# Optimization experiments

Hardware: AMD Instinct MI355X
Metric: run time of the kernel (lower is better)

Reference implementation:

```python
import jax, jax.numpy as jnp
import numpy as np

N_NODES = 20000
N_EDGES = 320000
INDIM = 64
OUTDIM = 128
EDGE_DIM = 16
HEADS = 4
ED = OUTDIM // 2          # encoded edge dim = 64
C1 = 2 * INDIM // HEADS   # 32 -> concat 128
C2 = OUTDIM // HEADS      # 32 -> concat 128
C3 = 2 * OUTDIM // HEADS  # 64 -> concat 256


def setup_inputs() -> dict:
    key = jax.random.key(0)
    ks = iter(jax.random.split(key, 80))
    def p(*shape):
        return jax.random.normal(next(ks), shape, dtype=jnp.float32) * 0.05
    inp = {}
    inp['x_in'] = jax.random.normal(next(ks), (N_NODES, INDIM), dtype=jnp.float32)
    inp['edge_index'] = jax.random.randint(next(ks), (2, N_EDGES), 0, N_NODES)
    inp['edge_attr'] = jax.random.normal(next(ks), (N_EDGES, EDGE_DIM), dtype=jnp.float32)
    # BatchNorm1d (eval mode: running stats)
    inp['bn0_g'] = jnp.ones(INDIM, jnp.float32) + p(INDIM)
    inp['bn0_b'] = p(INDIM)
    inp['bn0_m'] = p(INDIM)
    inp['bn0_v'] = jnp.ones(INDIM, jnp.float32) + 0.1 * jax.random.uniform(next(ks), (INDIM,))
    # edge encoder: Linear(edge_dim,outdim) -> LeakyReLU -> Linear(outdim,outdim//2) -> LeakyReLU
    inp['ee_W1'] = p(EDGE_DIM, OUTDIM); inp['ee_b1'] = p(OUTDIM)
    inp['ee_W2'] = p(OUTDIM, ED); inp['ee_b2'] = p(ED)
    # GATv2 layers: lin_l, lin_r (bias), lin_edge (no bias), att [H,C], out bias [H*C]
    def gat_params(prefix, din, C):
        inp[prefix + '_Wl'] = p(din, HEADS * C); inp[prefix + '_bl'] = p(HEADS * C)
        inp[prefix + '_Wr'] = p(din, HEADS * C); inp[prefix + '_br'] = p(HEADS * C)
        inp[prefix + '_We'] = p(ED, HEADS * C)
        inp[prefix + '_att'] = p(HEADS, C)
        inp[prefix + '_bias'] = p(HEADS * C)
    gat_params('g1', INDIM, C1)
    gat_params('g2', HEADS * C1, C2)
    gat_params('g3', HEADS * C2, C3)
    # LayerNorms
    inp['ln1_g'] = jnp.ones(HEADS * C1, jnp.float32); inp['ln1_b'] = p(HEADS * C1)
    inp['ln2_g'] = jnp.ones(HEADS * C2, jnp.float32); inp['ln2_b'] = p(HEADS * C2)
    inp['ln3_g'] = jnp.ones(HEADS * C3, jnp.float32); inp['ln3_b'] = p(HEADS * C3)
    # skip / mixing / heads
    inp['skip_W'] = p(INDIM, HEADS * C1); inp['skip_b'] = p(HEADS * C1)
    inp['alpha_p'] = jnp.float32(0.3)
    inp['fp_W'] = p(HEADS * C1, HEADS * C3); inp['fp_b'] = p(HEADS * C3)
    catout = HEADS * C3
    inp['np_W1'] = p(catout, catout // 2); inp['np_b1'] = p(catout // 2)
    inp['np_W2'] = p(catout // 2, catout // 4); inp['np_b2'] = p(catout // 4)
    inp['np_W3'] = p(catout // 4, 1); inp['np_b3'] = p(1)
    return inp


def _ln(x, g, b):
    m = jnp.mean(x, axis=-1, keepdims=True)
    v = jnp.var(x, axis=-1, keepdims=True)
    return (x - m) / jnp.sqrt(v + 1e-5) * g + b


def _gatv2(x, src, dst, ea, Wl, bl, Wr, br, We, att, bias, N):
    # GATv2Conv (eval): e = att . leaky_relu(x_j + x_i + e_ij, 0.2); segment softmax over dst
    H, C = att.shape
    xl = (x @ Wl + bl).reshape(N, H, C)   # source transform
    xr = (x @ Wr + br).reshape(N, H, C)   # target transform
    ee = (ea @ We).reshape(-1, H, C)      # edge transform (no bias)
    m = jax.nn.leaky_relu(xl[src] + xr[dst] + ee, 0.2)  # [E,H,C]
    e = jnp.einsum('ehc,hc->eh', m, att)
    emax = jax.ops.segment_max(e, dst, num_segments=N)
    ex = jnp.exp(e - emax[dst])
    den = jax.ops.segment_sum(ex, dst, num_segments=N)
    alpha = ex / (den[dst] + 1e-16)       # [E,H]
    out = jax.ops.segment_sum(xl[src] * alpha[:, :, None], dst, num_segments=N)
    return out.reshape(N, H * C) + bias, alpha


def reference(x_in, edge_index, edge_attr, bn0_g, bn0_b, bn0_m, bn0_v,
              ee_W1, ee_b1, ee_W2, ee_b2,
              g1_Wl, g1_bl, g1_Wr, g1_br, g1_We, g1_att, g1_bias,
              g2_Wl, g2_bl, g2_Wr, g2_br, g2_We, g2_att, g2_bias,
              g3_Wl, g3_bl, g3_Wr, g3_br, g3_We, g3_att, g3_bias,
              ln1_g, ln1_b, ln2_g, ln2_b, ln3_g, ln3_b,
              skip_W, skip_b, alpha_p, fp_W, fp_b,
              np_W1, np_b1, np_W2, np_b2, np_W3, np_b3):
    N = x_in.shape[0]
    # BatchNorm1d eval
    x = (x_in - bn0_m) / jnp.sqrt(bn0_v + 1e-5) * bn0_g + bn0_b
    # edge encoder + L2 normalize
    ea = jax.nn.leaky_relu(edge_attr @ ee_W1 + ee_b1, 0.01)
    ea = jax.nn.leaky_relu(ea @ ee_W2 + ee_b2, 0.01)
    ea = ea / jnp.maximum(jnp.linalg.norm(ea, axis=-1, keepdims=True), 1e-12)
    # add self loops (fill_value='mean' of incoming encoded edge_attr)
    src0, dst0 = edge_index[0], edge_index[1]
    deg = jax.ops.segment_sum(jnp.ones_like(ea[:, 0]), dst0, num_segments=N)
    loop_attr = jax.ops.segment_sum(ea, dst0, num_segments=N) / jnp.maximum(deg, 1.0)[:, None]
    ar = jnp.arange(N, dtype=src0.dtype)
    src = jnp.concatenate([src0, ar]); dst = jnp.concatenate([dst0, ar])
    ea2 = jnp.concatenate([ea, loop_attr], axis=0)
    x1, a1 = _gatv2(x, src, dst, ea2, g1_Wl, g1_bl, g1_Wr, g1_br, g1_We, g1_att, g1_bias, N)
    x1 = jax.nn.leaky_relu(_ln(x1, ln1_g, ln1_b), 0.01)
    skip1 = 0.01 * (x @ skip_W + skip_b) + x1  # skip_weight = 0.01 (frozen)
    x2, a2 = _gatv2(skip1, src, dst, ea2, g2_Wl, g2_bl, g2_Wr, g2_br, g2_We, g2_att, g2_bias, N)
    x2 = jax.nn.leaky_relu(_ln(x2, ln2_g, ln2_b), 0.01)
    x3, a3 = _gatv2(x2, src, dst, ea2, g3_Wl, g3_bl, g3_Wr, g3_br, g3_We, g3_att, g3_bias, N)
    x3 = jax.nn.leaky_relu(_ln(x3, ln3_g, ln3_b), 0.01)
    s = jax.nn.sigmoid(alpha_p)
    xf = s * (x1 @ fp_W + fp_b) + (1.0 - s) * x3
    h = jax.nn.elu(xf @ np_W1 + np_b1)
    h = jax.nn.elu(h @ np_W2 + np_b2)
    node_probs = h @ np_W3 + np_b3
    return (xf, node_probs, a1, a2, a3)
```

## Files before the change

### kernel.cpp

```cpp
#include <hip/hip_runtime.h>
#include <math.h>

#define DEV __device__ __forceinline__

typedef __attribute__((ext_vector_type(8))) short bf16x8;
typedef __attribute__((ext_vector_type(4))) float f32x4;

DEV float leakyf(float x, float s) { return x > 0.f ? x : s * x; }

DEV unsigned short f2bf(float f) {
  unsigned u = __float_as_uint(f);
  unsigned r = (u + 0x7fff + ((u >> 16) & 1)) >> 16;
  return (unsigned short)r;
}
DEV float bf2f(unsigned short h) { return __uint_as_float((unsigned)h << 16); }

DEV float sel4(float4 v, int h) {
  float a = (h & 1) ? v.y : v.x;
  float b = (h & 1) ? v.w : v.z;
  return (h & 2) ? b : a;
}

DEV float wave_sum(float v) {
#pragma unroll
  for (int o = 1; o < 64; o <<= 1) v += __shfl_xor(v, o);
  return v;
}
DEV float wave_max(float v) {
#pragma unroll
  for (int o = 1; o < 64; o <<= 1) v = fmaxf(v, __shfl_xor(v, o));
  return v;
}

struct WJob { const float* in; unsigned short* out; int K; int Nc; };
struct WJobs { WJob j[13]; };

__global__ __launch_bounds__(256) void wt_kernel(WJobs jobs) {
  WJob jb = jobs.j[blockIdx.y];
  int total = jb.K * jb.Nc;
  for (int i = blockIdx.x * 256 + threadIdx.x; i < total; i += gridDim.x * 256) {
    int c = i / jb.K, k = i - c * jb.K;
    jb.out[i] = f2bf(jb.in[(size_t)k * jb.Nc + c]);
  }
}

__global__ __launch_bounds__(256) void bn_kernel(
    const float* __restrict__ xin, const float* __restrict__ g,
    const float* __restrict__ b, const float* __restrict__ m,
    const float* __restrict__ v, float* __restrict__ xout, int total) {
  int i = blockIdx.x * 256 + threadIdx.x;
  if (i < total) {
    int c = i & 63;
    xout[i] = (xin[i] - m[c]) * rsqrtf(v[c] + 1e-5f) * g[c] + b[c];
  }
}

__global__ __launch_bounds__(256, 2) void edge_enc_kernel(
    const float* __restrict__ edge_attr, const unsigned short* __restrict__ WT1,
    const float* __restrict__ b1, const unsigned short* __restrict__ WT2,
    const float* __restrict__ b2, unsigned short* __restrict__ ea_bf, int E) {
  __shared__ unsigned short sEa1[64][136];
  int tid = threadIdx.x, lane = tid & 63, w = tid >> 6;
  int g = lane >> 4, q = lane & 15;
  bf16x8 w1f[8];
#pragma unroll
  for (int t = 0; t < 8; t++) {
    bf16x8 v = {};
    if (g < 2) v = *(const bf16x8*)(WT1 + (size_t)(16 * t + q) * 16 + 8 * g);
    w1f[t] = v;
  }
  float b1v[8];
#pragma unroll
  for (int t = 0; t < 8; t++) b1v[t] = b1[16 * t + q];
  bf16x8 w2f[4][4];
#pragma unroll
  for (int t = 0; t < 4; t++)
#pragma unroll
    for (int kc = 0; kc < 4; kc++)
      w2f[t][kc] = *(const bf16x8*)(WT2 + (size_t)(16 * t + q) * 128 + 32 * kc + 8 * g);
  float b2v[4];
#pragma unroll
  for (int t = 0; t < 4; t++) b2v[t] = b2[16 * t + q];

  int gstride = gridDim.x * 64;

  auto load_attr = [&](int base) -> bf16x8 {
    bf16x8 af = {};
    if (g < 2) {
      int e = base + w * 16 + q;
      if (e >= E) e = E - 1;
      const float* ap = edge_attr + (size_t)e * 16 + 8 * g;
      float4 x0 = *(const float4*)ap;
      float4 x1 = *(const float4*)(ap + 4);
      af[0] = (short)f2bf(x0.x); af[1] = (short)f2bf(x0.y);
      af[2] = (short)f2bf(x0.z); af[3] = (short)f2bf(x0.w);
      af[4] = (short)f2bf(x1.x); af[5] = (short)f2bf(x1.y);
      af[6] = (short)f2bf(x1.z); af[7] = (short)f2bf(x1.w);
    }
    return af;
  };

  int base = blockIdx.x * 64;
  if (base >= E) return;
  bf16x8 af = load_attr(base);
  for (; base < E; ) {
    int next = base + gstride;
    bf16x8 af_next = {};
    if (next < E) af_next = load_attr(next);
    int e0 = base + w * 16;
    f32x4 acc1[8];
#pragma unroll
    for (int t = 0; t < 8; t++) acc1[t] = (f32x4){0.f, 0.f, 0.f, 0.f};
#pragma unroll
    for (int t = 0; t < 8; t++)
      acc1[t] = __builtin_amdgcn_mfma_f32_16x16x32_bf16(af, w1f[t], acc1[t], 0, 0, 0);
#pragma unroll
    for (int t = 0; t < 8; t++)
#pragma unroll
      for (int r = 0; r < 4; r++) {
        float v = leakyf(acc1[t][r] + b1v[t], 0.01f);
        sEa1[w * 16 + g * 4 + r][16 * t + q] = f2bf(v);
      }
    f32x4 acc2[4];
#pragma unroll
    for (int t = 0; t < 4; t++) acc2[t] = (f32x4){0.f, 0.f, 0.f, 0.f};
#pragma unroll
    for (int kc = 0; kc < 4; kc++) {
      bf16x8 a2 = *(const bf16x8*)&sEa1[w * 16 + q][32 * kc + 8 * g];
#pragma unroll
      for (int t = 0; t < 4; t++)
        acc2[t] = __builtin_amdgcn_mfma_f32_16x16x32_bf16(a2, w2f[t][kc], acc2[t], 0, 0, 0);
    }
#pragma unroll
    for (int r = 0; r < 4; r++) {
      float vv[4];
      float p = 0.f;
#pragma unroll
      for (int t = 0; t < 4; t++) {
        float v = leakyf(acc2[t][r] + b2v[t], 0.01f);
        vv[t] = v;
        p += v * v;
      }
#pragma unroll
      for (int o = 1; o < 16; o <<= 1) p += __shfl_xor(p, o);
      float sc = 1.f / fmaxf(sqrtf(p), 1e-12f);
      int e = e0 + g * 4 + r;
      if (e < E) {
#pragma unroll
        for (int t = 0; t < 4; t++)
          ea_bf[(size_t)e * 64 + 16 * t + q] = f2bf(vv[t] * sc);
      }
    }
    af = af_next;
    base = next;
  }
}

__global__ __launch_bounds__(256) void count_kernel(const int* __restrict__ dst0,
                                                    int* __restrict__ counts, int E, int E2) {
  int i = blockIdx.x * 256 + threadIdx.x;
  if (i < E2) {
    int d = (i < E) ? dst0[i] : (i - E);
    atomicAdd(&counts[d], 1);
  }
}

__global__ __launch_bounds__(1024) void scan_kernel(const int* __restrict__ counts,
                                                    int* __restrict__ rowptr,
                                                    int* __restrict__ fill, int N) {
  __shared__ int part[1024];
  int tid = threadIdx.x;
  int chunk = (N + 1023) / 1024;
  int lo = tid * chunk, hi = lo + chunk;
  if (hi > N) hi = N;
  if (lo > N) lo = N;
  int s = 0;
  for (int i = lo; i < hi; i++) s += counts[i];
  part[tid] = s;
  __syncthreads();
#pragma unroll
  for (int o = 1; o < 1024; o <<= 1) {
    int v = (tid >= o) ? part[tid - o] : 0;
    __syncthreads();
    part[tid] += v;
    __syncthreads();
  }
  if (tid == 1023) rowptr[N] = part[1023];
  int off = part[tid] - s;
  for (int i = lo; i < hi; i++) {
    rowptr[i] = off;
    fill[i] = off;
    off += counts[i];
  }
}

__global__ __launch_bounds__(256) void fill_kernel(const int* __restrict__ src0,
                                                   const int* __restrict__ dst0,
                                                   int* __restrict__ fill,
                                                   int* __restrict__ csr,
                                                   int* __restrict__ srcpos,
                                                   int* __restrict__ dstpos, int E, int E2) {
  int i = blockIdx.x * 256 + threadIdx.x;
  if (i < E2) {
    int d, s;
    if (i < E) {
      d = dst0[i];
      s = src0[i];
    } else {
      d = s = i - E;
    }
    int pos = atomicAdd(&fill[d], 1);
    csr[pos] = i;
    srcpos[pos] = s;
    dstpos[pos] = d;
  }
}

__global__ __launch_bounds__(256) void loopattr_kernel(unsigned short* __restrict__ ea_bf,
                                                       const int* __restrict__ rowptr,
                                                       const int* __restrict__ csr, int N, int E) {
  int lane = threadIdx.x & 63, wv = threadIdx.x >> 6;
  int stride = gridDim.x * 4;
  for (int n = blockIdx.x * 4 + wv; n < N; n += stride) {
    int r0 = rowptr[n], r1 = rowptr[n + 1];
    float acc = 0.f;
    int cnt = 0;
    for (int i = r0; i < r1; i++) {
      int e = csr[i];
      if (e < E) {
        acc += bf2f(ea_bf[(size_t)e * 64 + lane]);
        cnt++;
      }
    }
    ea_bf[((size_t)E + n) * 64 + lane] = f2bf(acc / fmaxf((float)cnt, 1.f));
  }
}

template <int MODE>
__global__ __launch_bounds__(256) void gemm_mfma_kernel(
    const float* __restrict__ A, const unsigned short* __restrict__ BT,
    const float* __restrict__ bias, void* __restrict__ Cout, int M, int K, int Nc,
    const float* __restrict__ aux, const float* __restrict__ alpha_p) {
  __shared__ unsigned short sA[64][40];
  __shared__ unsigned short sB[64][40];
  int tid = threadIdx.x, lane = tid & 63, w = tid >> 6;
  int g = lane >> 4, q = lane & 15;
  int bm = blockIdx.y * 64, bn = blockIdx.x * 64;
  f32x4 acc[4];
#pragma unroll
  for (int t = 0; t < 4; t++) acc[t] = (f32x4){0.f, 0.f, 0.f, 0.f};
  int r = tid >> 2, ko = (tid & 3) * 8;
  for (int k0 = 0; k0 < K; k0 += 32) {
    {
      int gm = bm + r;
      bf16x8 v = {};
      if (gm < M) {
        const float* ap = A + (size_t)gm * K + k0 + ko;
        float4 x0 = *(const float4*)ap;
        float4 x1 = *(const float4*)(ap + 4);
        v[0] = (short)f2bf(x0.x); v[1] = (short)f2bf(x0.y);
        v[2] = (short)f2bf(x0.z); v[3] = (short)f2bf(x0.w);
        v[4] = (short)f2bf(x1.x); v[5] = (short)f2bf(x1.y);
        v[6] = (short)f2bf(x1.z); v[7] = (short)f2bf(x1.w);
      }
      *(bf16x8*)&sA[r][ko] = v;
      int gc = bn + r;
      bf16x8 bv = {};
      if (gc < Nc) bv = *(const bf16x8*)(BT + (size_t)gc * K + k0 + ko);
      *(bf16x8*)&sB[r][ko] = bv;
    }
    __syncthreads();
    bf16x8 a = *(const bf16x8*)&sA[w * 16 + q][8 * g];
#pragma unroll
    for (int t = 0; t < 4; t++) {
      bf16x8 b = *(const bf16x8*)&sB[16 * t + q][8 * g];
      acc[t] = __builtin_amdgcn_mfma_f32_16x16x32_bf16(a, b, acc[t], 0, 0, 0);
    }
    __syncthreads();
  }
  float s = 0.f;
  if (MODE == 3) s = 1.f / (1.f + __expf(-alpha_p[0]));
#pragma unroll
  for (int t = 0; t < 4; t++) {
    int col = bn + 16 * t + q;
#pragma unroll
    for (int rr = 0; rr < 4; rr++) {
      int row = bm + w * 16 + g * 4 + rr;
      if (row < M && col < Nc) {
        float v = acc[t][rr] + bias[col];
        if (MODE == 2) v = v > 0.f ? v : (__expf(v) - 1.f);
        if (MODE == 3) v = s * v + (1.f - s) * aux[(size_t)row * Nc + col];
        if (MODE == 1)
          ((unsigned short*)Cout)[(size_t)row * Nc + col] = f2bf(v);
        else
          ((float*)Cout)[(size_t)row * Nc + col] = v;
      }
    }
  }
}

struct GJob { const unsigned short* BT; const float* bias; void* out; int mode; };
struct GJobs { GJob j[3]; };

__global__ __launch_bounds__(256) void gemm_mfma_batched(
    const float* __restrict__ A, GJobs jobs, int M, int K, int Nc) {
  __shared__ unsigned short sA[64][40];
  __shared__ unsigned short sB[64][40];
  GJob jb = jobs.j[blockIdx.z];
  const unsigned short* BT = jb.BT;
  int tid = threadIdx.x, lane = tid & 63, w = tid >> 6;
  int g = lane >> 4, q = lane & 15;
  int bm = blockIdx.y * 64, bn = blockIdx.x * 64;
  f32x4 acc[4];
#pragma unroll
  for (int t = 0; t < 4; t++) acc[t] = (f32x4){0.f, 0.f, 0.f, 0.f};
  int r = tid >> 2, ko = (tid & 3) * 8;
  for (int k0 = 0; k0 < K; k0 += 32) {
    {
      int gm = bm + r;
      bf16x8 v = {};
      if (gm < M) {
        const float* ap = A + (size_t)gm * K + k0 + ko;
        float4 x0 = *(const float4*)ap;
        float4 x1 = *(const float4*)(ap + 4);
        v[0] = (short)f2bf(x0.x); v[1] = (short)f2bf(x0.y);
        v[2] = (short)f2bf(x0.z); v[3] = (short)f2bf(x0.w);
        v[4] = (short)f2bf(x1.x); v[5] = (short)f2bf(x1.y);
        v[6] = (short)f2bf(x1.z); v[7] = (short)f2bf(x1.w);
      }
      *(bf16x8*)&sA[r][ko] = v;
      int gc = bn + r;
      bf16x8 bv = {};
      if (gc < Nc) bv = *(const bf16x8*)(BT + (size_t)gc * K + k0 + ko);
      *(bf16x8*)&sB[r][ko] = bv;
    }
    __syncthreads();
    bf16x8 a = *(const bf16x8*)&sA[w * 16 + q][8 * g];
#pragma unroll
    for (int t = 0; t < 4; t++) {
      bf16x8 b = *(const bf16x8*)&sB[16 * t + q][8 * g];
      acc[t] = __builtin_amdgcn_mfma_f32_16x16x32_bf16(a, b, acc[t], 0, 0, 0);
    }
    __syncthreads();
  }
#pragma unroll
  for (int t = 0; t < 4; t++) {
    int col = bn + 16 * t + q;
#pragma unroll
    for (int rr = 0; rr < 4; rr++) {
      int row = bm + w * 16 + g * 4 + rr;
      if (row < M && col < Nc) {
        float v = acc[t][rr] + jb.bias[col];
        if (jb.mode == 1)
          ((unsigned short*)jb.out)[(size_t)row * Nc + col] = f2bf(v);
        else
          ((float*)jb.out)[(size_t)row * Nc + col] = v;
      }
    }
  }
}

template <int C, bool SPLIT>
__global__ __launch_bounds__(256) void score_mfma_kernel(
    const unsigned short* __restrict__ ea_bf, const unsigned short* __restrict__ xl,
    const unsigned short* __restrict__ xr, const float* __restrict__ We,
    const float* __restrict__ att, const int* __restrict__ csr,
    const int* __restrict__ srcpos, const int* __restrict__ dstpos,
    float* __restrict__ e_s, int E2, int HCfull, int col_off_in) {
  int lane = threadIdx.x & 63;
  int wv = threadIdx.x >> 6;
  int g = lane >> 4, q = lane & 15;
  int col_off = SPLIT ? (wv & 1) * 128 : col_off_in;
  bf16x8 bfrag[8][2];
#pragma unroll
  for (int t = 0; t < 8; t++)
#pragma unroll
    for (int kc = 0; kc < 2; kc++) {
      bf16x8 bv;
#pragma unroll
      for (int j = 0; j < 8; j++) {
        int k = kc * 32 + g * 8 + j;
        bv[j] = (short)f2bf(We[(size_t)k * HCfull + col_off + 16 * t + q]);
      }
      bfrag[t][kc] = bv;
    }
  float attv[8];
#pragma unroll
  for (int t = 0; t < 8; t++) attv[t] = att[col_off + 16 * t + q];

  constexpr int TPH = C / 16;
  constexpr int NH = 8 / TPH;
  const int headbase = col_off / C;

  int tiles = (E2 + 15) / 16;
  int tstart = SPLIT ? (blockIdx.x * 2 + (wv >> 1)) : (blockIdx.x * 4 + wv);
  int nw = SPLIT ? (gridDim.x * 2) : (gridDim.x * 4);
  for (int tile = tstart; tile < tiles; tile += nw) {
    int i0 = tile * 16;
    int ia = i0 + q;
    if (ia >= E2) ia = E2 - 1;
    int erow = csr[ia];
    const unsigned short* ap = ea_bf + (size_t)erow * 64 + g * 8;
    bf16x8 a0 = *(const bf16x8*)(ap);
    bf16x8 a1 = *(const bf16x8*)(ap + 32);
    f32x4 acc[8];
#pragma unroll
    for (int t = 0; t < 8; t++) acc[t] = (f32x4){0.f, 0.f, 0.f, 0.f};
#pragma unroll
    for (int t = 0; t < 8; t++) {
      acc[t] = __builtin_amdgcn_mfma_f32_16x16x32_bf16(a0, bfrag[t][0], acc[t], 0, 0, 0);
      acc[t] = __builtin_amdgcn_mfma_f32_16x16x32_bf16(a1, bfrag[t][1], acc[t], 0, 0, 0);
    }
    int sn[4], dn[4];
#pragma unroll
    for (int r = 0; r < 4; r++) {
      int i = i0 + g * 4 + r;
      if (i >= E2) i = E2 - 1;
      sn[r] = srcpos[i];
      dn[r] = dstpos[i];
    }
    float p[NH][4];
#pragma unroll
    for (int hh = 0; hh < NH; hh++)
#pragma unroll
      for (int r = 0; r < 4; r++) p[hh][r] = 0.f;
#pragma unroll
    for (int t = 0; t < 8; t++) {
      int col = col_off + 16 * t + q;
#pragma unroll
      for (int r = 0; r < 4; r++) {
        float xv = bf2f(xl[(size_t)sn[r] * HCfull + col]) +
                   bf2f(xr[(size_t)dn[r] * HCfull + col]) + acc[t][r];
        xv = xv > 0.f ? xv : 0.2f * xv;
        p[t / TPH][r] += xv * attv[t];
      }
    }
#pragma unroll
    for (int hh = 0; hh < NH; hh++)
#pragma unroll
      for (int r = 0; r < 4; r++) {
#pragma unroll
        for (int o = 1; o < 16; o <<= 1) p[hh][r] += __shfl_xor(p[hh][r], o);
      }
    if (q == 0) {
#pragma unroll
      for (int r = 0; r < 4; r++) {
        int i = i0 + g * 4 + r;
        if (i < E2) {
#pragma unroll
          for (int hh = 0; hh < NH; hh++)
            e_s[(size_t)i * 4 + headbase + hh] = p[hh][r];
        }
      }
    }
  }
}

template <int HC, bool L1MODE>
__global__ __launch_bounds__(256) void aggr_kernel(
    const float* __restrict__ e_s, const unsigned short* __restrict__ xl,
    const int* __restrict__ rowptr, const int* __restrict__ srcpos,
    const float* __restrict__ bias,
    const float* __restrict__ lng, const float* __restrict__ lnb,
    float* __restrict__ xout,
    float* __restrict__ x1out, const float* __restrict__ skipproj,
    float* __restrict__ md, int N) {
  constexpr int CPL = HC / 64;
  int lane = threadIdx.x & 63, wv = threadIdx.x >> 6;
  int stride = gridDim.x * 4;
  const float4* e_s4 = (const float4*)e_s;
  for (int n = blockIdx.x * 4 + wv; n < N; n += stride) {
    int r0 = rowptr[n], r1 = rowptr[n + 1];
    float m0 = -1e30f, m1 = -1e30f, m2 = -1e30f, m3 = -1e30f;
    for (int i = r0 + lane; i < r1; i += 64) {
      float4 v = e_s4[i];
      m0 = fmaxf(m0, v.x);
      m1 = fmaxf(m1, v.y);
      m2 = fmaxf(m2, v.z);
      m3 = fmaxf(m3, v.w);
    }
    m0 = wave_max(m0);
    m1 = wave_max(m1);
    m2 = wave_max(m2);
    m3 = wave_max(m3);
    float d0 = 0.f, d1 = 0.f, d2 = 0.f, d3 = 0.f;
    for (int i = r0 + lane; i < r1; i += 64) {
      float4 v = e_s4[i];
      d0 += __expf(v.x - m0);
      d1 += __expf(v.y - m1);
      d2 += __expf(v.z - m2);
      d3 += __expf(v.w - m3);
    }
    d0 = wave_sum(d0);
    d1 = wave_sum(d1);
    d2 = wave_sum(d2);
    d3 = wave_sum(d3);
    float i0 = 1.f / (d0 + 1e-16f), i1 = 1.f / (d1 + 1e-16f);
    float i2 = 1.f / (d2 + 1e-16f), i3 = 1.f / (d3 + 1e-16f);
    if (lane == 0) {
      float* mp = md + (size_t)n * 8;
      mp[0] = m0; mp[1] = m1; mp[2] = m2; mp[3] = m3;
      mp[4] = i0; mp[5] = i1; mp[6] = i2; mp[7] = i3;
    }
    int h = lane >> 4;
    float mh = (h & 2) ? ((h & 1) ? m3 : m2) : ((h & 1) ? m1 : m0);
    float ih = (h & 2) ? ((h & 1) ? i3 : i2) : ((h & 1) ? i1 : i0);
    float acc[CPL];
#pragma unroll
    for (int j = 0; j < CPL; j++) acc[j] = 0.f;
    int c0 = lane * CPL;
    int i = r0;
    for (; i + 4 <= r1; i += 4) {
      float sh0, sh1, sh2, sh3;
      int sn0, sn1, sn2, sn3;
      {
        float4 a = e_s4[i], b = e_s4[i + 1], c = e_s4[i + 2], d = e_s4[i + 3];
        sh0 = sel4(a, h); sh1 = sel4(b, h); sh2 = sel4(c, h); sh3 = sel4(d, h);
      }
      sn0 = srcpos[i]; sn1 = srcpos[i + 1]; sn2 = srcpos[i + 2]; sn3 = srcpos[i + 3];
      if constexpr (CPL == 2) {
        ushort2 t0 = *(const ushort2*)(xl + (size_t)sn0 * HC + c0);
        ushort2 t1 = *(const ushort2*)(xl + (size_t)sn1 * HC + c0);
        ushort2 t2 = *(const ushort2*)(xl + (size_t)sn2 * HC + c0);
        ushort2 t3 = *(const ushort2*)(xl + (size_t)sn3 * HC + c0);
        float a0 = __expf(sh0 - mh) * ih;
        float a1 = __expf(sh1 - mh) * ih;
        float a2 = __expf(sh2 - mh) * ih;
        float a3 = __expf(sh3 - mh) * ih;
        acc[0] += a0 * bf2f(t0.x) + a1 * bf2f(t1.x) + a2 * bf2f(t2.x) + a3 * bf2f(t3.x);
        acc[1] += a0 * bf2f(t0.y) + a1 * bf2f(t1.y) + a2 * bf2f(t2.y) + a3 * bf2f(t3.y);
      } else {
        ushort4 t0 = *(const ushort4*)(xl + (size_t)sn0 * HC + c0);
        ushort4 t1 = *(const ushort4*)(xl + (size_t)sn1 * HC + c0);
        ushort4 t2 = *(const ushort4*)(xl + (size_t)sn2 * HC + c0);
        ushort4 t3 = *(const ushort4*)(xl + (size_t)sn3 * HC + c0);
        float a0 = __expf(sh0 - mh) * ih;
        float a1 = __expf(sh1 - mh) * ih;
        float a2 = __expf(sh2 - mh) * ih;
        float a3 = __expf(sh3 - mh) * ih;
        acc[0] += a0 * bf2f(t0.x) + a1 * bf2f(t1.x) + a2 * bf2f(t2.x) + a3 * bf2f(t3.x);
        acc[1] += a0 * bf2f(t0.y) + a1 * bf2f(t1.y) + a2 * bf2f(t2.y) + a3 * bf2f(t3.y);
        acc[2] += a0 * bf2f(t0.z) + a1 * bf2f(t1.z) + a2 * bf2f(t2.z) + a3 * bf2f(t3.z);
        acc[3] += a0 * bf2f(t0.w) + a1 * bf2f(t1.w) + a2 * bf2f(t2.w) + a3 * bf2f(t3.w);
      }
    }
    for (; i < r1; i++) {
      float sh = sel4(e_s4[i], h);
      float a = __expf(sh - mh) * ih;
      int sn = srcpos[i];
      const unsigned short* xp = xl + (size_t)sn * HC + c0;
      if constexpr (CPL == 2) {
        ushort2 t = *(const ushort2*)xp;
        acc[0] += a * bf2f(t.x);
        acc[1] += a * bf2f(t.y);
      } else {
        ushort4 t = *(const ushort4*)xp;
        acc[0] += a * bf2f(t.x);
        acc[1] += a * bf2f(t.y);
        acc[2] += a * bf2f(t.z);
        acc[3] += a * bf2f(t.w);
      }
    }
    float vals[CPL];
    float vs = 0.f, vq = 0.f;
#pragma unroll
    for (int j = 0; j < CPL; j++) {
      float t = acc[j] + bias[c0 + j];
      vals[j] = t;
      vs += t;
      vq += t * t;
    }
    vs = wave_sum(vs);
    vq = wave_sum(vq);
    float mean = vs * (1.f / HC);
    float var = vq * (1.f / HC) - mean * mean;
    float rstd = rsqrtf(fmaxf(var, 0.f) + 1e-5f);
#pragma unroll
    for (int j = 0; j < CPL; j++) {
      int c = c0 + j;
      float y = (vals[j] - mean) * rstd * lng[c] + lnb[c];
      y = leakyf(y, 0.01f);
      if constexpr (L1MODE) {
        x1out[(size_t)n * HC + c] = y;
        xout[(size_t)n * HC + c] = 0.01f * skipproj[(size_t)n * HC + c] + y;
      } else {
        xout[(size_t)n * HC + c] = y;
      }
    }
  }
}

__global__ __launch_bounds__(256) void alpha_kernel(
    const float* __restrict__ e_s, const int* __restrict__ csr,
    const int* __restrict__ dstpos, const float* __restrict__ md,
    float* __restrict__ alpha_out, int E2) {
  int i = blockIdx.x * 256 + threadIdx.x;
  if (i < E2) {
    float4 sv = ((const float4*)e_s)[i];
    int d = dstpos[i];
    const float* mp = md + (size_t)d * 8;
    float4 a;
    a.x = __expf(sv.x - mp[0]) * mp[4];
    a.y = __expf(sv.y - mp[1]) * mp[5];
    a.z = __expf(sv.z - mp[2]) * mp[6];
    a.w = __expf(sv.w - mp[3]) * mp[7];
    ((float4*)alpha_out)[csr[i]] = a;
  }
}

extern "C" void kernel_launch(void* const* d_in, const int* in_sizes, int n_in,
                              void* d_out, int out_size, void* d_ws, size_t ws_size,
                              hipStream_t stream) {
  (void)n_in;
  (void)out_size;
  (void)ws_size;
  const float* x_in = (const float*)d_in[0];
  const int* edge_index = (const int*)d_in[1];
  const float* edge_attr = (const float*)d_in[2];
  const float* bn0_g = (const float*)d_in[3];
  const float* bn0_b = (const float*)d_in[4];
  const float* bn0_m = (const float*)d_in[5];
  const float* bn0_v = (const float*)d_in[6];
  const float* eeW1 = (const float*)d_in[7];
  const float* eeb1 = (const float*)d_in[8];
  const float* eeW2 = (const float*)d_in[9];
  const float* eeb2 = (const float*)d_in[10];
  const float* g1_Wl = (const float*)d_in[11];
  const float* g1_bl = (const float*)d_in[12];
  const float* g1_Wr = (const float*)d_in[13];
  const float* g1_br = (const float*)d_in[14];
  const float* g1_We = (const float*)d_in[15];
  const float* g1_att = (const float*)d_in[16];
  const float* g1_bias = (const float*)d_in[17];
  const float* g2_Wl = (const float*)d_in[18];
  const float* g2_bl = (const float*)d_in[19];
  const float* g2_Wr = (const float*)d_in[20];
  const float* g2_br = (const float*)d_in[21];
  const float* g2_We = (const float*)d_in[22];
  const float* g2_att = (const float*)d_in[23];
  const float* g2_bias = (const float*)d_in[24];
  const float* g3_Wl = (const float*)d_in[25];
  const float* g3_bl = (const float*)d_in[26];
  const float* g3_Wr = (const float*)d_in[27];
  const float* g3_br = (const float*)d_in[28];
  const float* g3_We = (const float*)d_in[29];
  const float* g3_att = (const float*)d_in[30];
  const float* g3_bias = (const float*)d_in[31];
  const float* ln1_g = (const float*)d_in[32];
  const float* ln1_b = (const float*)d_in[33];
  const float* ln2_g = (const float*)d_in[34];
  const float* ln2_b = (const float*)d_in[35];
  const float* ln3_g = (const float*)d_in[36];
  const float* ln3_b = (const float*)d_in[37];
  const float* skip_W = (const float*)d_in[38];
  const float* skip_b = (const float*)d_in[39];
  const float* alpha_p = (const float*)d_in[40];
  const float* fp_W = (const float*)d_in[41];
  const float* fp_b = (const float*)d_in[42];
  const float* np_W1 = (const float*)d_in[43];
  const float* np_b1 = (const float*)d_in[44];
  const float* np_W2 = (const float*)d_in[45];
  const float* np_b2 = (const float*)d_in[46];
  const float* np_W3 = (const float*)d_in[47];
  const float* np_b3 = (const float*)d_in[48];

  const int N = in_sizes[0] / 64;
  const int E = in_sizes[2] / 16;
  const int E2 = E + N;
  const int* src0 = edge_index;
  const int* dst0 = edge_index + E;

  float* ws = (float*)d_ws;
  size_t off = 0;
  float* x = ws + off;         off += (size_t)N * 64;
  unsigned short* ea_bf = (unsigned short*)(ws + off); off += (size_t)E2 * 32;
  unsigned short* xl = (unsigned short*)(ws + off);    off += (size_t)N * 128;
  unsigned short* xr = (unsigned short*)(ws + off);    off += (size_t)N * 128;
  float* skipproj = ws + off;  off += (size_t)N * 128;
  float* x1 = ws + off;        off += (size_t)N * 128;
  float* skip1 = ws + off;     off += (size_t)N * 128;
  float* x2 = ws + off;        off += (size_t)N * 128;
  float* x3 = ws + off;        off += (size_t)N * 256;
  float* e_s = ws + off;       off += (size_t)E2 * 4;
  float* h2 = ws + off;        off += (size_t)N * 64;
  float* md = ws + off;        off += (size_t)N * 8;
  int* counts = (int*)(ws + off);
  int* rowptr = counts + N;
  int* fill = rowptr + N + 1;
  int* csr = fill + N;
  int* srcpos = csr + E2;
  int* dstpos = srcpos + E2;
  off += (size_t)(3 * N + 1 + 3 * E2);
  off = (off + 3) & ~(size_t)3;
  unsigned short* wtp = (unsigned short*)(ws + off);
  auto alloc_wt = [&](int elems) {
    unsigned short* p = wtp;
    wtp += (elems + 7) & ~7;
    return p;
  };
  unsigned short* wt_g1l = alloc_wt(64 * 128);
  unsigned short* wt_g1r = alloc_wt(64 * 128);
  unsigned short* wt_skip = alloc_wt(64 * 128);
  unsigned short* wt_g2l = alloc_wt(128 * 128);
  unsigned short* wt_g2r = alloc_wt(128 * 128);
  unsigned short* wt_g3l = alloc_wt(128 * 256);
  unsigned short* wt_g3r = alloc_wt(128 * 256);
  unsigned short* wt_fp = alloc_wt(128 * 256);
  unsigned short* wt_np1 = alloc_wt(256 * 128);
  unsigned short* wt_np2 = alloc_wt(128 * 64);
  unsigned short* wt_np3 = alloc_wt(64 * 1);
  unsigned short* wt_ee1 = alloc_wt(16 * 128);
  unsigned short* wt_ee2 = alloc_wt(128 * 64);

  float* out = (float*)d_out;
  float* xf = out;
  float* npout = out + (size_t)N * 256;
  float* a1 = npout + N;
  float* a2 = a1 + (size_t)E2 * 4;
  float* a3 = a2 + (size_t)E2 * 4;

  WJobs jobs;
  jobs.j[0] = {g1_Wl, wt_g1l, 64, 128};
  jobs.j[1] = {g1_Wr, wt_g1r, 64, 128};
  jobs.j[2] = {skip_W, wt_skip, 64, 128};
  jobs.j[3] = {g2_Wl, wt_g2l, 128, 128};
  jobs.j[4] = {g2_Wr, wt_g2r, 128, 128};
  jobs.j[5] = {g3_Wl, wt_g3l, 128, 256};
  jobs.j[6] = {g3_Wr, wt_g3r, 128, 256};
  jobs.j[7] = {fp_W, wt_fp, 128, 256};
  jobs.j[8] = {np_W1, wt_np1, 256, 128};
  jobs.j[9] = {np_W2, wt_np2, 128, 64};
  jobs.j[10] = {np_W3, wt_np3, 64, 1};
  jobs.j[11] = {eeW1, wt_ee1, 16, 128};
  jobs.j[12] = {eeW2, wt_ee2, 128, 64};

  hipMemsetAsync(counts, 0, (size_t)N * sizeof(int), stream);
  wt_kernel<<<dim3(64, 13), 256, 0, stream>>>(jobs);
  bn_kernel<<<(N * 64 + 255) / 256, 256, 0, stream>>>(x_in, bn0_g, bn0_b, bn0_m, bn0_v, x, N * 64);
  edge_enc_kernel<<<1280, 256, 0, stream>>>(edge_attr, wt_ee1, eeb1, wt_ee2, eeb2, ea_bf, E);
  count_kernel<<<(E2 + 255) / 256, 256, 0, stream>>>(dst0, counts, E, E2);
  scan_kernel<<<1, 1024, 0, stream>>>(counts, rowptr, fill, N);
  fill_kernel<<<(E2 + 255) / 256, 256, 0, stream>>>(src0, dst0, fill, csr, srcpos, dstpos, E, E2);
  loopattr_kernel<<<(N + 3) / 4, 256, 0, stream>>>(ea_bf, rowptr, csr, N, E);

  auto gemm = [&](int mode, const float* A, const unsigned short* BT, const float* bias,
                  void* Cp, int M, int K, int Nc, const float* aux) {
    dim3 gdim((Nc + 63) / 64, (M + 63) / 64);
    switch (mode) {
      case 0: gemm_mfma_kernel<0><<<gdim, 256, 0, stream>>>(A, BT, bias, Cp, M, K, Nc, nullptr, nullptr); break;
      case 2: gemm_mfma_kernel<2><<<gdim, 256, 0, stream>>>(A, BT, bias, Cp, M, K, Nc, nullptr, nullptr); break;
      case 3: gemm_mfma_kernel<3><<<gdim, 256, 0, stream>>>(A, BT, bias, Cp, M, K, Nc, aux, alpha_p); break;
    }
  };
  auto gemm_batch = [&](const float* A, int M, int K, int Nc, GJobs gj, int nz) {
    dim3 gdim((Nc + 63) / 64, (M + 63) / 64, nz);
    gemm_mfma_batched<<<gdim, 256, 0, stream>>>(A, gj, M, K, Nc);
  };

  const int nblk_node = (N + 3) / 4;
  const int score_blocks = 1024;
  const int nblk_edge = (E2 + 255) / 256;

  {
    GJobs gj;
    gj.j[0] = {wt_g1l, g1_bl, xl, 1};
    gj.j[1] = {wt_g1r, g1_br, xr, 1};
    gj.j[2] = {wt_skip, skip_b, skipproj, 0};
    gemm_batch(x, N, 64, 128, gj, 3);
  }
  score_mfma_kernel<32, false><<<score_blocks, 256, 0, stream>>>(ea_bf, xl, xr, g1_We, g1_att, csr, srcpos, dstpos, e_s, E2, 128, 0);
  aggr_kernel<128, true><<<nblk_node, 256, 0, stream>>>(e_s, xl, rowptr, srcpos, g1_bias, ln1_g, ln1_b,
                                                        skip1, x1, skipproj, md, N);
  alpha_kernel<<<nblk_edge, 256, 0, stream>>>(e_s, csr, dstpos, md, a1, E2);
  {
    GJobs gj;
    gj.j[0] = {wt_g2l, g2_bl, xl, 1};
    gj.j[1] = {wt_g2r, g2_br, xr, 1};
    gj.j[2] = {nullptr, nullptr, nullptr, 0};
    gemm_batch(skip1, N, 128, 128, gj, 2);
  }
  score_mfma_kernel<32, false><<<score_blocks, 256, 0, stream>>>(ea_bf, xl, xr, g2_We, g2_att, csr, srcpos, dstpos, e_s, E2, 128, 0);
  aggr_kernel<128, false><<<nblk_node, 256, 0, stream>>>(e_s, xl, rowptr, srcpos, g2_bias, ln2_g, ln2_b,
                                                         x2, nullptr, nullptr, md, N);
  alpha_kernel<<<nblk_edge, 256, 0, stream>>>(e_s, csr, dstpos, md, a2, E2);
  {
    GJobs gj;
    gj.j[0] = {wt_g3l, g3_bl, xl, 1};
    gj.j[1] = {wt_g3r, g3_br, xr, 1};
    gj.j[2] = {nullptr, nullptr, nullptr, 0};
    gemm_batch(x2, N, 128, 256, gj, 2);
  }
  score_mfma_kernel<64, true><<<score_blocks, 256, 0, stream>>>(ea_bf, xl, xr, g3_We, g3_att, csr, srcpos, dstpos, e_s, E2, 256, 0);
  aggr_kernel<256, false><<<nblk_node, 256, 0, stream>>>(e_s, xl, rowptr, srcpos, g3_bias, ln3_g, ln3_b,
                                                         x3, nullptr, nullptr, md, N);
  alpha_kernel<<<nblk_edge, 256, 0, stream>>>(e_s, csr, dstpos, md, a3, E2);
  gemm(3, x1, wt_fp, fp_b, xf, N, 128, 256, x3);
  gemm(2, xf, wt_np1, np_b1, skipproj, N, 256, 128, nullptr);
  gemm(2, skipproj, wt_np2, np_b2, h2, N, 128, 64, nullptr);
  gemm(0, h2, wt_np3, np_b3, npout, N, 64, 1, nullptr);
}
```

Measured before the change: 505.7 us.

## Store encoded edge features in CSR order to make score loads contiguous

```diff
diff --git a/kernel.cpp b/kernel.cpp
--- a/kernel.cpp
+++ b/kernel.cpp
@@ -58,7 +58,8 @@
 __global__ __launch_bounds__(256, 2) void edge_enc_kernel(
     const float* __restrict__ edge_attr, const unsigned short* __restrict__ WT1,
     const float* __restrict__ b1, const unsigned short* __restrict__ WT2,
-    const float* __restrict__ b2, unsigned short* __restrict__ ea_bf, int E) {
+    const float* __restrict__ b2, unsigned short* __restrict__ ea_csr,
+    const int* __restrict__ inv, int E) {
   __shared__ unsigned short sEa1[64][136];
   int tid = threadIdx.x, lane = tid & 63, w = tid >> 6;
   int g = lane >> 4, q = lane & 15;
@@ -146,9 +147,10 @@
       float sc = 1.f / fmaxf(sqrtf(p), 1e-12f);
       int e = e0 + g * 4 + r;
       if (e < E) {
+        int pos = inv[e];
 #pragma unroll
         for (int t = 0; t < 4; t++)
-          ea_bf[(size_t)e * 64 + 16 * t + q] = f2bf(vv[t] * sc);
+          ea_csr[(size_t)pos * 64 + 16 * t + q] = f2bf(vv[t] * sc);
       }
     }
     af = af_next;
@@ -199,7 +201,8 @@
                                                    int* __restrict__ fill,
                                                    int* __restrict__ csr,
                                                    int* __restrict__ srcpos,
-                                                   int* __restrict__ dstpos, int E, int E2) {
+                                                   int* __restrict__ dstpos,
+                                                   int* __restrict__ inv, int E, int E2) {
   int i = blockIdx.x * 256 + threadIdx.x;
   if (i < E2) {
     int d, s;
@@ -213,10 +216,11 @@
     csr[pos] = i;
     srcpos[pos] = s;
     dstpos[pos] = d;
-  }
-}
-
-__global__ __launch_bounds__(256) void loopattr_kernel(unsigned short* __restrict__ ea_bf,
+    inv[i] = pos;
+  }
+}
+
+__global__ __launch_bounds__(256) void loopattr_kernel(unsigned short* __restrict__ ea_csr,
                                                        const int* __restrict__ rowptr,
                                                        const int* __restrict__ csr, int N, int E) {
   int lane = threadIdx.x & 63, wv = threadIdx.x >> 6;
@@ -224,15 +228,17 @@
   for (int n = blockIdx.x * 4 + wv; n < N; n += stride) {
     int r0 = rowptr[n], r1 = rowptr[n + 1];
     float acc = 0.f;
-    int cnt = 0;
+    int loop_pos = r0;
     for (int i = r0; i < r1; i++) {
       int e = csr[i];
       if (e < E) {
-        acc += bf2f(ea_bf[(size_t)e * 64 + lane]);
-        cnt++;
-      }
-    }
-    ea_bf[((size_t)E + n) * 64 + lane] = f2bf(acc / fmaxf((float)cnt, 1.f));
+        acc += bf2f(ea_csr[(size_t)i * 64 + lane]);
+      } else {
+        loop_pos = i;
+      }
+    }
+    int cnt = r1 - r0 - 1;
+    ea_csr[(size_t)loop_pos * 64 + lane] = f2bf(acc / fmaxf((float)cnt, 1.f));
   }
 }
 
@@ -362,10 +368,10 @@
 
 template <int C, bool SPLIT>
 __global__ __launch_bounds__(256) void score_mfma_kernel(
-    const unsigned short* __restrict__ ea_bf, const unsigned short* __restrict__ xl,
+    const unsigned short* __restrict__ ea_csr, const unsigned short* __restrict__ xl,
     const unsigned short* __restrict__ xr, const float* __restrict__ We,
-    const float* __restrict__ att, const int* __restrict__ csr,
-    const int* __restrict__ srcpos, const int* __restrict__ dstpos,
+    const float* __restrict__ att, const int* __restrict__ srcpos,
+    const int* __restrict__ dstpos,
     float* __restrict__ e_s, int E2, int HCfull, int col_off_in) {
   int lane = threadIdx.x & 63;
   int wv = threadIdx.x >> 6;
@@ -399,8 +405,7 @@
     int i0 = tile * 16;
     int ia = i0 + q;
     if (ia >= E2) ia = E2 - 1;
-    int erow = csr[ia];
-    const unsigned short* ap = ea_bf + (size_t)erow * 64 + g * 8;
+    const unsigned short* ap = ea_csr + (size_t)ia * 64 + g * 8;
     bf16x8 a0 = *(const bf16x8*)(ap);
     bf16x8 a1 = *(const bf16x8*)(ap + 32);
     f32x4 acc[8];
@@ -673,7 +678,7 @@
   float* ws = (float*)d_ws;
   size_t off = 0;
   float* x = ws + off;         off += (size_t)N * 64;
-  unsigned short* ea_bf = (unsigned short*)(ws + off); off += (size_t)E2 * 32;
+  unsigned short* ea_csr = (unsigned short*)(ws + off); off += (size_t)E2 * 32;
   unsigned short* xl = (unsigned short*)(ws + off);    off += (size_t)N * 128;
   unsigned short* xr = (unsigned short*)(ws + off);    off += (size_t)N * 128;
   float* skipproj = ws + off;  off += (size_t)N * 128;
@@ -690,7 +695,8 @@
   int* csr = fill + N;
   int* srcpos = csr + E2;
   int* dstpos = srcpos + E2;
-  off += (size_t)(3 * N + 1 + 3 * E2);
+  int* inv = dstpos + E2;
+  off += (size_t)(3 * N + 1 + 4 * E2);
   off = (off + 3) & ~(size_t)3;
   unsigned short* wtp = (unsigned short*)(ws + off);
   auto alloc_wt = [&](int elems) {
@@ -737,11 +743,11 @@
   hipMemsetAsync(counts, 0, (size_t)N * sizeof(int), stream);
   wt_kernel<<<dim3(64, 13), 256, 0, stream>>>(jobs);
   bn_kernel<<<(N * 64 + 255) / 256, 256, 0, stream>>>(x_in, bn0_g, bn0_b, bn0_m, bn0_v, x, N * 64);
-  edge_enc_kernel<<<1280, 256, 0, stream>>>(edge_attr, wt_ee1, eeb1, wt_ee2, eeb2, ea_bf, E);
   count_kernel<<<(E2 + 255) / 256, 256, 0, stream>>>(dst0, counts, E, E2);
   scan_kernel<<<1, 1024, 0, stream>>>(counts, rowptr, fill, N);
-  fill_kernel<<<(E2 + 255) / 256, 256, 0, stream>>>(src0, dst0, fill, csr, srcpos, dstpos, E, E2);
-  loopattr_kernel<<<(N + 3) / 4, 256, 0, stream>>>(ea_bf, rowptr, csr, N, E);
+  fill_kernel<<<(E2 + 255) / 256, 256, 0, stream>>>(src0, dst0, fill, csr, srcpos, dstpos, inv, E, E2);
+  edge_enc_kernel<<<1280, 256, 0, stream>>>(edge_attr, wt_ee1, eeb1, wt_ee2, eeb2, ea_csr, inv, E);
+  loopattr_kernel<<<(N + 3) / 4, 256, 0, stream>>>(ea_csr, rowptr, csr, N, E);
 
   auto gemm = [&](int mode, const float* A, const unsigned short* BT, const float* bias,
                   void* Cp, int M, int K, int Nc, const float* aux) {
@@ -768,7 +774,7 @@
     gj.j[2] = {wt_skip, skip_b, skipproj, 0};
     gemm_batch(x, N, 64, 128, gj, 3);
   }
-  score_mfma_kernel<32, false><<<score_blocks, 256, 0, stream>>>(ea_bf, xl, xr, g1_We, g1_att, csr, srcpos, dstpos, e_s, E2, 128, 0);
+  score_mfma_kernel<32, false><<<score_blocks, 256, 0, stream>>>(ea_csr, xl, xr, g1_We, g1_att, srcpos, dstpos, e_s, E2, 128, 0);
   aggr_kernel<128, true><<<nblk_node, 256, 0, stream>>>(e_s, xl, rowptr, srcpos, g1_bias, ln1_g, ln1_b,
                                                         skip1, x1, skipproj, md, N);
   alpha_kernel<<<nblk_edge, 256, 0, stream>>>(e_s, csr, dstpos, md, a1, E2);
@@ -779,7 +785,7 @@
     gj.j[2] = {nullptr, nullptr, nullptr, 0};
     gemm_batch(skip1, N, 128, 128, gj, 2);
   }
-  score_mfma_kernel<32, false><<<score_blocks, 256, 0, stream>>>(ea_bf, xl, xr, g2_We, g2_att, csr, srcpos, dstpos, e_s, E2, 128, 0);
+  score_mfma_kernel<32, false><<<score_blocks, 256, 0, stream>>>(ea_csr, xl, xr, g2_We, g2_att, srcpos, dstpos, e_s, E2, 128, 0);
   aggr_kernel<128, false><<<nblk_node, 256, 0, stream>>>(e_s, xl, rowptr, srcpos, g2_bias, ln2_g, ln2_b,
                                                          x2, nullptr, nullptr, md, N);
   alpha_kernel<<<nblk_edge, 256, 0, stream>>>(e_s, csr, dstpos, md, a2, E2);
@@ -790,7 +796,7 @@
     gj.j[2] = {nullptr, nullptr, nullptr, 0};
     gemm_batch(x2, N, 128, 256, gj, 2);
   }
-  score_mfma_kernel<64, true><<<score_blocks, 256, 0, stream>>>(ea_bf, xl, xr, g3_We, g3_att, csr, srcpos, dstpos, e_s, E2, 256, 0);
+  score_mfma_kernel<64, true><<<score_blocks, 256, 0, stream>>>(ea_csr, xl, xr, g3_We, g3_att, srcpos, dstpos, e_s, E2, 256, 0);
   aggr_kernel<256, false><<<nblk_node, 256, 0, stream>>>(e_s, xl, rowptr, srcpos, g3_bias, ln3_g, ln3_b,
                                                          x3, nullptr, nullptr, md, N);
   alpha_kernel<<<nblk_edge, 256, 0, stream>>>(e_s, csr, dstpos, md, a3, E2);
```

Result: no change. 505.9 us (median of 2 runs) (+0.0%).
